# Kernel optimization log

Hardware: AMD Instinct MI355X
Metric: run time of the kernel (lower is better)

## Reference

```python
import jax, jax.numpy as jnp
import numpy as np

T, N, C_IN, M, ORDER = 16384, 16, 2, 3, 3
S = M * ORDER + ORDER + 1  # 13 weights per (out_ch, in_ch)


def setup_inputs() -> dict:
    key = jax.random.key(0)
    ks = jax.random.split(key, 6)
    return {
        "inputs": jax.random.normal(ks[0], (T, N, C_IN), jnp.float32),
        "a_list": jax.random.uniform(ks[1], (M, N, N), jnp.float32),  # positive -> valid D^{-1/2}
        "gcn_wx": 0.25 * jax.random.normal(ks[2], (T, C_IN, S), jnp.float32),
        "gcn_bx": jnp.zeros((T, N), jnp.float32),
        "gcn_wh": 0.25 * jax.random.normal(ks[3], (T, 1, S), jnp.float32),
        "gcn_bh": jnp.zeros((T, N), jnp.float32),
        "gru_k": 0.25 * jax.random.normal(ks[4], (T, 6, N, N), jnp.float32),  # Wr,Ur,Wz,Uz,Wh,Uh kernels
        "gru_b": jnp.zeros((T, 6, N), jnp.float32),
    }


def _laplacians(a_list):
    # Per motif: D = diag(colsum(A)); L = D - A; L_hat = D^{-1/2} L D^{-1/2}
    d = jnp.sum(a_list, axis=1)                      # [M,N] column sums (tf.reduce_sum axis=0)
    L = jax.vmap(jnp.diag)(d) - a_list               # [M,N,N]
    dis = 1.0 / jnp.sqrt(d)                          # diag of inv(sqrt(D))
    return dis[:, :, None] * L * dis[:, None, :]     # [M,N,N]


def _gcn(x, L_hats, W, b):
    # x: [N,C]; W: [C,S]; b: [N]. Chebyshev-style polynomial per input channel.
    I = jnp.eye(N, dtype=x.dtype)

    def per_channel(w):  # w: [S]
        ws = w[M * ORDER + 1] * I
        P = I
        for k in range(1, ORDER):
            coeffs = jnp.stack([w[l * (k - 1)] for l in range(M)])  # faithful odd indexing
            P = jnp.einsum('l,lij,jk->ik', coeffs, L_hats, P)
            ws = ws + w[M * ORDER + k + 1] * P
        return ws  # [N,N]

    WS = jax.vmap(per_channel)(W)                    # [C,N,N]
    out = jnp.einsum('cnm,mc->n', WS, x)             # sum_c WS[c] @ x[:,c]
    return jax.nn.relu(out + b)                      # [N] (N == 16 == bias width)


def _gru(x, h, K, B):
    # x, h: [N]; K: [6,N,N]; B: [6,N]
    r = jax.nn.sigmoid(x @ K[0] + B[0] + h @ K[1] + B[1])
    z = jax.nn.sigmoid(x @ K[2] + B[2] + h @ K[3] + B[3])
    hc = jnp.tanh(x @ K[4] + B[4] + (r * h) @ K[5] + B[5])
    return z * h + (1.0 - z) * hc


def reference(inputs, a_list, gcn_wx, gcn_bx, gcn_wh, gcn_bh, gru_k, gru_b):
    L_hats = _laplacians(a_list)

    # t == 0: hidden GCN branch is zeros
    xg0 = _gcn(inputs[0], L_hats, gcn_wx[0], gcn_bx[0])
    h0 = _gru(xg0, jnp.zeros((N,), inputs.dtype), gru_k[0], gru_b[0])

    def step(h_prev, per_t):
        x_t, wx, bx, wh, bh, K, B = per_t
        xg = _gcn(x_t, L_hats, wx, bx)
        hg = _gcn(h_prev[:, None], L_hats, wh, bh)   # hidden treated as [N,1] features
        h_t = _gru(xg, hg, K, B)
        return h_t, h_t

    xs = (inputs[1:], gcn_wx[1:], gcn_bx[1:], gcn_wh[1:], gcn_bh[1:], gru_k[1:], gru_b[1:])
    _, hs = jax.lax.scan(step, h0, xs)
    return jnp.concatenate([h0[None], hs], axis=0)   # [T, N]
```

## Files before the change

### kernel.cpp

```cpp
#include <hip/hip_runtime.h>

#define TT 16384
#define W_WARM 416
#define CHUNK 16
#define NSTEP (W_WARM + CHUNK)
#define RECF 1088
#define RECB 4352

#define RL(v, m) __int_as_float(__builtin_amdgcn_readlane(__float_as_int(v), (m)))
#define ROR(v, K) \
    __int_as_float(__builtin_amdgcn_update_dpp(0, __float_as_int(v), 0x120 + (K), 0xF, 0xF, false))

__device__ __forceinline__ float fsig(float x) {
    return __builtin_amdgcn_rcpf(1.0f + __builtin_amdgcn_exp2f(-1.4426950408889634f * x));
}
__device__ __forceinline__ float ftanh(float x) {
    return fmaf(-2.0f, __builtin_amdgcn_rcpf(1.0f + __builtin_amdgcn_exp2f(2.8853900817779268f * x)), 1.0f);
}

__global__ void k_fixed(const float* __restrict__ a, float* __restrict__ fix) {
    __shared__ float Lh[3][16][16];
    __shared__ float Ls[16][16];
    __shared__ float dsh[3][16];
    int tid = threadIdx.x;
    if (tid < 48) {
        int l = tid >> 4, j = tid & 15;
        float s = 0.f;
        for (int i = 0; i < 16; i++) s += a[l * 256 + i * 16 + j];
        dsh[l][j] = s;
    }
    __syncthreads();
    int i = tid >> 4, j = tid & 15;
    for (int l = 0; l < 3; l++) {
        float L = ((i == j) ? dsh[l][i] : 0.0f) - a[l * 256 + i * 16 + j];
        Lh[l][i][j] = L * rsqrtf(dsh[l][i]) * rsqrtf(dsh[l][j]);
    }
    __syncthreads();
    float ls = Lh[0][i][j] + Lh[1][i][j] + Lh[2][i][j];
    Ls[i][j] = ls;
    fix[i * 16 + j] = ls;
    __syncthreads();
    for (int l = 0; l < 3; l++) {
        float m = 0.f;
        for (int k = 0; k < 16; k++) m += Lh[l][i][k] * Ls[k][j];
        fix[(l + 1) * 256 + i * 16 + j] = m;
    }
}

__global__ __launch_bounds__(128) void k_prep3(const float* __restrict__ inp,
                                               const float* __restrict__ wx_,
                                               const float* __restrict__ bx_,
                                               const float* __restrict__ wh_,
                                               const float* __restrict__ bh_,
                                               const float* __restrict__ gk,
                                               const float* __restrict__ gb,
                                               float* __restrict__ ws) {
    __shared__ float sfix[1024];
    __shared__ float srec[8][RECF];
    __shared__ float sgk[8][768];
    __shared__ float sxg[8][16];
    int tid = threadIdx.x;
    int t_base = blockIdx.x * 8;
    for (int i = tid; i < 1024; i += 128) sfix[i] = ws[i];
    {
        float4* dst = (float4*)&sgk[0][0];
        const float4* src = (const float4*)gk;
        for (int i = tid; i < 1536; i += 128) {
            int tl2 = i / 192, r = i - tl2 * 192;
            int mtx = r >> 6, w = r & 63;
            dst[i] = src[(size_t)(t_base + tl2) * 384 + mtx * 128 + w];
        }
    }
    __syncthreads();
    int tl = tid >> 4, n = tid & 15;
    int t = t_base + tl;
    bool z0 = (t == 0);

    const float* wh = wh_ + t * 13;
    float w0 = wh[0];
    float aI = wh[10], aL = wh[11] * w0;
    float wc = wh[12] * w0;
    float c0 = wc * w0, c1 = wc * wh[1], c2 = wc * wh[2];
    for (int m = 0; m < 16; m++) {
        float Av = aL * sfix[n * 16 + m] + c0 * sfix[256 + n * 16 + m] +
                   c1 * sfix[512 + n * 16 + m] + c2 * sfix[768 + n * 16 + m];
        if (m == n) Av += aI;
        srec[tl][n * 16 + ((n - m) & 15)] = z0 ? 0.f : Av;
    }

    float acc = bx_[t * 16 + n];
    for (int c = 0; c < 2; c++) {
        const float* wx = wx_ + t * 26 + c * 13;
        float yL = 0.f, y0 = 0.f, y1 = 0.f, y2 = 0.f;
        for (int m = 0; m < 16; m++) {
            float xm = inp[t * 32 + m * 2 + c];
            yL += sfix[n * 16 + m] * xm;
            y0 += sfix[256 + n * 16 + m] * xm;
            y1 += sfix[512 + n * 16 + m] * xm;
            y2 += sfix[768 + n * 16 + m] * xm;
        }
        float xn = inp[t * 32 + n * 2 + c];
        float b0 = wx[12] * wx[0];
        acc += wx[10] * xn + wx[11] * wx[0] * yL + b0 * (wx[0] * y0 + wx[1] * y1 + wx[2] * y2);
    }
    float xg = fmaxf(acc, 0.f);
    sxg[tl][n] = xg;
    __syncthreads();

    const float* gbt = gb + (size_t)t * 96;
    float u[3];
    for (int qq = 0; qq < 3; qq++) {
        const float* K = &sgk[tl][qq * 256];
        float s = gbt[2 * qq * 16 + n] + gbt[(2 * qq + 1) * 16 + n];
        for (int m = 0; m < 16; m++) s += sxg[tl][m] * K[m * 16 + n];
        u[qq] = s;
    }
    srec[tl][1024 + n * 4 + 0] = z0 ? 0.f : bh_[t * 16 + n];
    srec[tl][1024 + n * 4 + 1] = u[0];
    srec[tl][1024 + n * 4 + 2] = u[1];
    srec[tl][1024 + n * 4 + 3] = u[2];
    __syncthreads();
    {
        float4* dst = (float4*)&sgk[0][0];
        const float4* src = (const float4*)gk;
        for (int i = tid; i < 1536; i += 128) {
            int tl2 = i / 192, r = i - tl2 * 192;
            int mtx = r >> 6, w = r & 63;
            dst[i] = src[(size_t)(t_base + tl2) * 384 + mtx * 128 + 64 + w];
        }
    }
    __syncthreads();
    for (int b = 0; b < 3; b++) {
        const float* K = &sgk[tl][b * 256];
        float* d = &srec[tl][256 * (b + 1)];
        for (int m = 0; m < 16; m++)
            d[n * 16 + ((n - m) & 15)] = K[m * 16 + n];
    }
    __syncthreads();
    float4* gdst = (float4*)(ws + 1024 + (size_t)t_base * RECF);
    const float4* lsrc = (const float4*)&srec[0][0];
    for (int i = tid; i < 8 * RECF / 4; i += 128) gdst[i] = lsrc[i];
}

struct Slot {
    float4 A0, A1, A2, A3;
    float4 B0, B1, B2, B3;
    float4 Z0, Z1, Z2, Z3;
    float4 C0, C1, C2, C3;
    float4 ex;
};

__device__ __forceinline__ void rot16(float v, float rr[16]) {
    rr[0] = v;
    rr[1] = ROR(v, 1);
    rr[2] = ROR(v, 2);
    rr[3] = ROR(v, 3);
    rr[4] = ROR(v, 4);
    rr[5] = ROR(v, 5);
    rr[6] = ROR(v, 6);
    rr[7] = ROR(v, 7);
    rr[8] = ROR(v, 8);
    rr[9] = ROR(v, 9);
    rr[10] = ROR(v, 10);
    rr[11] = ROR(v, 11);
    rr[12] = ROR(v, 12);
    rr[13] = ROR(v, 13);
    rr[14] = ROR(v, 14);
    rr[15] = ROR(v, 15);
}

__device__ __forceinline__ float dotw(const float4& w0, const float4& w1, const float4& w2,
                                      const float4& w3, const float rr[16]) {
    float a0 = w0.x * rr[0];
    float a1 = w0.y * rr[1];
    float a2 = w0.z * rr[2];
    float a3 = w0.w * rr[3];
    a0 = fmaf(w1.x, rr[4], a0);
    a1 = fmaf(w1.y, rr[5], a1);
    a2 = fmaf(w1.z, rr[6], a2);
    a3 = fmaf(w1.w, rr[7], a3);
    a0 = fmaf(w2.x, rr[8], a0);
    a1 = fmaf(w2.y, rr[9], a1);
    a2 = fmaf(w2.z, rr[10], a2);
    a3 = fmaf(w2.w, rr[11], a3);
    a0 = fmaf(w3.x, rr[12], a0);
    a1 = fmaf(w3.y, rr[13], a1);
    a2 = fmaf(w3.z, rr[14], a2);
    a3 = fmaf(w3.w, rr[15], a3);
    return (a0 + a1) + (a2 + a3);
}

__device__ __forceinline__ void load_slot(Slot& S, const char* __restrict__ recb8, int t,
                                          unsigned offA, unsigned offX) {
    const char* r = recb8 + (size_t)t * RECB;
    S.A0 = *(const float4*)(r + offA);
    S.A1 = *(const float4*)(r + offA + 16);
    S.A2 = *(const float4*)(r + offA + 32);
    S.A3 = *(const float4*)(r + offA + 48);
    S.B0 = *(const float4*)(r + offA + 1024);
    S.B1 = *(const float4*)(r + offA + 1040);
    S.B2 = *(const float4*)(r + offA + 1056);
    S.B3 = *(const float4*)(r + offA + 1072);
    S.Z0 = *(const float4*)(r + offA + 2048);
    S.Z1 = *(const float4*)(r + offA + 2064);
    S.Z2 = *(const float4*)(r + offA + 2080);
    S.Z3 = *(const float4*)(r + offA + 2096);
    S.C0 = *(const float4*)(r + offA + 3072);
    S.C1 = *(const float4*)(r + offA + 3088);
    S.C2 = *(const float4*)(r + offA + 3104);
    S.C3 = *(const float4*)(r + offA + 3120);
    S.ex = *(const float4*)(r + offX);
}

__device__ __forceinline__ float wstep6(const Slot& S, float hv, int t, int t0, int n,
                                        float* __restrict__ out) {
    float hh[16];
    rot16(hv, hh);
    float hg = fmaxf(dotw(S.A0, S.A1, S.A2, S.A3, hh) + S.ex.x, 0.f);
    float hgr[16];
    rot16(hg, hgr);
    float r = fsig(dotw(S.B0, S.B1, S.B2, S.B3, hgr) + S.ex.y);
    float z = fsig(dotw(S.Z0, S.Z1, S.Z2, S.Z3, hgr) + S.ex.z);
    float rg[16];
    rot16(r * hg, rg);
    float hc = ftanh(dotw(S.C0, S.C1, S.C2, S.C3, rg) + S.ex.w);
    float hn = fmaf(z, hg - hc, hc);
    if ((unsigned)(t - t0) < (unsigned)CHUNK) out[(size_t)t * 16 + n] = hn;
    return hn;
}

__global__ __launch_bounds__(64, 1) void k_walk6(const float* __restrict__ ws,
                                                 float* __restrict__ out) {
    const char* recb8 = (const char*)(ws + 1024);
    int lane = threadIdx.x;
    int n = lane & 15;
    int row = lane >> 4;

    unsigned offA = n * 64;
    unsigned offX = 4096 + n * 16;

    int b = blockIdx.x;
    int L = (b & 7) * 32 + (b >> 3);
    int t0 = (L * 4 + row) * CHUNK;
    int ts = t0 - W_WARM;
    if (ts < 0) ts = 0;
    int tend = t0 + CHUNK - 1;

    float hv = 0.f;

    Slot R0, R1, R2;
    load_slot(R0, recb8, ts + 0, offA, offX);
    load_slot(R1, recb8, ts + 1, offA, offX);
    load_slot(R2, recb8, ts + 2, offA, offX);

    for (int s = 0; s < NSTEP; s += 3) {
        int t = ts + s;
        int tl;
        hv = wstep6(R0, hv, t + 0, t0, n, out);
        tl = t + 3;
        if (tl > tend) tl = tend;
        load_slot(R0, recb8, tl, offA, offX);
        hv = wstep6(R1, hv, t + 1, t0, n, out);
        tl = t + 4;
        if (tl > tend) tl = tend;
        load_slot(R1, recb8, tl, offA, offX);
        hv = wstep6(R2, hv, t + 2, t0, n, out);
        tl = t + 5;
        if (tl > tend) tl = tend;
        load_slot(R2, recb8, tl, offA, offX);
    }
}

__global__ void k_prep_c(const float* __restrict__ inp, const float* __restrict__ wx_,
                         const float* __restrict__ bx_, const float* __restrict__ wh_,
                         const float* __restrict__ bh_, const float* __restrict__ gk,
                         const float* __restrict__ gb, float* __restrict__ ws) {
    __shared__ float sfix[1024];
    __shared__ float sxg[16][16];
    int tid = threadIdx.x;
    for (int idx = tid; idx < 1024; idx += 256) sfix[idx] = ws[idx];
    int tl = tid >> 4, n = tid & 15;
    int t = blockIdx.x * 16 + tl;
    __syncthreads();
    float* rec = ws + 1024 + (size_t)t * 320;
    bool z0 = (t == 0);
    const float* wh = wh_ + t * 13;
    float w0 = wh[0];
    float aI = wh[10], aL = wh[11] * w0;
    float wc = wh[12] * w0;
    float c0 = wc * w0, c1 = wc * wh[1], c2 = wc * wh[2];
    for (int m = 0; m < 16; m++) {
        float Av = aL * sfix[n * 16 + m] + c0 * sfix[256 + n * 16 + m] +
                   c1 * sfix[512 + n * 16 + m] + c2 * sfix[768 + n * 16 + m];
        if (m == n) Av += aI;
        rec[n * 16 + m] = z0 ? 0.f : Av;
    }
    float acc = bx_[t * 16 + n];
    for (int c = 0; c < 2; c++) {
        const float* wx = wx_ + t * 26 + c * 13;
        float yL = 0.f, y0 = 0.f, y1 = 0.f, y2 = 0.f;
        for (int m = 0; m < 16; m++) {
            float xm = inp[t * 32 + m * 2 + c];
            yL += sfix[n * 16 + m] * xm;
            y0 += sfix[256 + n * 16 + m] * xm;
            y1 += sfix[512 + n * 16 + m] * xm;
            y2 += sfix[768 + n * 16 + m] * xm;
        }
        float xn = inp[t * 32 + n * 2 + c];
        float b0 = wx[12] * wx[0];
        acc += wx[10] * xn + wx[11] * wx[0] * yL + b0 * (wx[0] * y0 + wx[1] * y1 + wx[2] * y2);
    }
    float xg = fmaxf(acc, 0.f);
    sxg[tl][n] = xg;
    __syncthreads();
    const float* Kb = gk + (size_t)t * 1536;
    const float* gbt = gb + (size_t)t * 96;
    for (int qq = 0; qq < 3; qq++) {
        const float* K = Kb + (2 * qq) * 256;
        float u = gbt[2 * qq * 16 + n] + gbt[(2 * qq + 1) * 16 + n];
        for (int m = 0; m < 16; m++) u += sxg[tl][m] * K[m * 16 + n];
        rec[256 + qq * 16 + n] = u;
    }
    rec[304 + n] = z0 ? 0.f : bh_[t * 16 + n];
}

struct RegsC {
    float WA[16], WB[16], WC[16];
    float uRZ, u4, bh;
};

__device__ __forceinline__ void load_step_c(const float* __restrict__ recb,
                                            const float* __restrict__ gk, int t, int n, int q,
                                            RegsC& R) {
    const float* rb = recb + (size_t)t * 320;
#pragma unroll
    for (int k = 0; k < 4; k++) ((float4*)R.WA)[k] = ((const float4*)(rb + n * 16))[k];
    const float* kb = gk + (size_t)t * 1536 + (1 + 2 * (q & 1)) * 256 + n;
    const float* kc = gk + (size_t)t * 1536 + 5 * 256 + n;
#pragma unroll
    for (int m = 0; m < 16; m++) {
        R.WB[m] = kb[m * 16];
        R.WC[m] = kc[m * 16];
    }
    R.uRZ = rb[256 + (q & 1) * 16 + n];
    R.u4 = rb[288 + n];
    R.bh = rb[304 + n];
}

__device__ __forceinline__ void wstep_c(const RegsC& R, float hs[16], int t, int t0, int lane,
                                        int n, float* __restrict__ out) {
    float a0 = 0.f, a1 = 0.f, a2 = 0.f, a3 = 0.f;
#pragma unroll
    for (int m = 0; m < 16; m += 4) {
        a0 = fmaf(R.WA[m + 0], hs[m + 0], a0);
        a1 = fmaf(R.WA[m + 1], hs[m + 1], a1);
        a2 = fmaf(R.WA[m + 2], hs[m + 2], a2);
        a3 = fmaf(R.WA[m + 3], hs[m + 3], a3);
    }
    float hg = fmaxf((a0 + a1) + (a2 + a3) + R.bh, 0.f);
    float hgs[16];
#pragma unroll
    for (int m = 0; m < 16; m++) hgs[m] = RL(hg, m);
    a0 = a1 = a2 = a3 = 0.f;
#pragma unroll
    for (int m = 0; m < 16; m += 4) {
        a0 = fmaf(R.WB[m + 0], hgs[m + 0], a0);
        a1 = fmaf(R.WB[m + 1], hgs[m + 1], a1);
        a2 = fmaf(R.WB[m + 2], hgs[m + 2], a2);
        a3 = fmaf(R.WB[m + 3], hgs[m + 3], a3);
    }
    float rz = fsig((a0 + a1) + (a2 + a3) + R.uRZ);
    float zsw = __shfl_xor(rz, 16);
    float rhg = rz * hg;
    float rhgs[16];
#pragma unroll
    for (int m = 0; m < 16; m++) rhgs[m] = RL(rhg, m);
    a0 = a1 = a2 = a3 = 0.f;
#pragma unroll
    for (int m = 0; m < 16; m += 4) {
        a0 = fmaf(R.WC[m + 0], rhgs[m + 0], a0);
        a1 = fmaf(R.WC[m + 1], rhgs[m + 1], a1);
        a2 = fmaf(R.WC[m + 2], rhgs[m + 2], a2);
        a3 = fmaf(R.WC[m + 3], rhgs[m + 3], a3);
    }
    float hc = ftanh((a0 + a1) + (a2 + a3) + R.u4);
    float h = fmaf(zsw, hg - hc, hc);
    if (t >= t0 && lane < 16) out[(size_t)t * 16 + n] = h;
#pragma unroll
    for (int m = 0; m < 16; m++) hs[m] = RL(h, m);
}

__global__ __launch_bounds__(64) void k_walk_c(const float* __restrict__ ws,
                                               const float* __restrict__ gk,
                                               float* __restrict__ out) {
    const float* recb = ws + 1024;
    int lane = threadIdx.x;
    int n = lane & 15;
    int q = lane >> 4;
    int t0 = blockIdx.x * 64;
    int te = t0 + 64;
    int ts = t0 - W_WARM;
    if (ts < 0) ts = 0;
    RegsC Ra, Rb;
    load_step_c(recb, gk, ts, n, q, Ra);
    load_step_c(recb, gk, ts + 1, n, q, Rb);
    float hs[16];
#pragma unroll
    for (int m = 0; m < 16; m++) hs[m] = 0.f;
    for (int t = ts; t < te; t += 2) {
        wstep_c(Ra, hs, t, t0, lane, n, out);
        int tn = t + 2;
        load_step_c(recb, gk, tn < TT ? tn : TT - 1, n, q, Ra);
        wstep_c(Rb, hs, t + 1, t0, lane, n, out);
        int tm = t + 3;
        load_step_c(recb, gk, tm < TT ? tm : TT - 1, n, q, Rb);
    }
}

extern "C" void kernel_launch(void* const* d_in, const int* in_sizes, int n_in, void* d_out,
                              int out_size, void* d_ws, size_t ws_size, hipStream_t stream) {
    const float* inp = (const float*)d_in[0];
    const float* a = (const float*)d_in[1];
    const float* wx = (const float*)d_in[2];
    const float* bx = (const float*)d_in[3];
    const float* wh = (const float*)d_in[4];
    const float* bh = (const float*)d_in[5];
    const float* gk = (const float*)d_in[6];
    const float* gb = (const float*)d_in[7];
    float* out = (float*)d_out;
    float* ws = (float*)d_ws;

    size_t need = 4ull * (1024ull + (size_t)TT * RECF);
    k_fixed<<<dim3(1), dim3(256), 0, stream>>>(a, ws);
    if (ws_size >= need) {
        k_prep3<<<dim3(TT / 8), dim3(128), 0, stream>>>(inp, wx, bx, wh, bh, gk, gb, ws);
        k_walk6<<<dim3(TT / (4 * CHUNK)), dim3(64), 0, stream>>>(ws, out);
    } else {
        k_prep_c<<<dim3(TT / 16), dim3(256), 0, stream>>>(inp, wx, bx, wh, bh, gk, gb, ws);
        k_walk_c<<<dim3(TT / 64), dim3(64), 0, stream>>>(ws, gk, out);
    }
}
```

Before: 506.7 us.

## Stream recurrence records through swizzled LDS ring with async global-to-LDS loads

Replaces direct global-to-register slot loads in the sequential walk with a 4-deep LDS ring filled by global_load_lds and read via ds_read_b128 with manual waitcnt control. Records are written with an XOR swizzle in prep to avoid LDS bank conflicts. Each block now walks two 32-step chains instead of four 16-step chains, reducing total redundant warmup work. Risks include fragile hand-tuned waitcnt counts and a slightly longer serial chain per block.

Result: no change. 500.8 us (-1.2%).

```diff
diff --git a/kernel.cpp b/kernel.cpp
--- a/kernel.cpp
+++ b/kernel.cpp
@@ -2,14 +2,22 @@
 
 #define TT 16384
 #define W_WARM 416
-#define CHUNK 16
+#define CHUNK 32
 #define NSTEP (W_WARM + CHUNK)
 #define RECF 1088
 #define RECB 4352
+#define NS 4
+#define SLOTF 2176
+#define SLOTB 8704
 
 #define RL(v, m) __int_as_float(__builtin_amdgcn_readlane(__float_as_int(v), (m)))
 #define ROR(v, K) \
     __int_as_float(__builtin_amdgcn_update_dpp(0, __float_as_int(v), 0x120 + (K), 0xF, 0xF, false))
+
+#define VMWAIT10() asm volatile("s_waitcnt vmcnt(10)")
+#define VMWAIT20() asm volatile("s_waitcnt vmcnt(20)")
+#define LGKMWAIT15() asm volatile("s_waitcnt lgkmcnt(15)")
+#define LAUNDER4(v) asm volatile("" : "+v"((v).x), "+v"((v).y), "+v"((v).z), "+v"((v).w))
 
 __device__ __forceinline__ float fsig(float x) {
     return __builtin_amdgcn_rcpf(1.0f + __builtin_amdgcn_exp2f(-1.4426950408889634f * x));
@@ -75,6 +83,7 @@
     int tl = tid >> 4, n = tid & 15;
     int t = t_base + tl;
     bool z0 = (t == 0);
+    int sw = (n >> 1) & 3;
 
     const float* wh = wh_ + t * 13;
     float w0 = wh[0];
@@ -85,7 +94,8 @@
         float Av = aL * sfix[n * 16 + m] + c0 * sfix[256 + n * 16 + m] +
                    c1 * sfix[512 + n * 16 + m] + c2 * sfix[768 + n * 16 + m];
         if (m == n) Av += aI;
-        srec[tl][n * 16 + ((n - m) & 15)] = z0 ? 0.f : Av;
+        int j = (n - m) & 15;
+        srec[tl][n * 16 + ((((j >> 2) ^ sw) << 2) | (j & 3))] = z0 ? 0.f : Av;
     }
 
     float acc = bx_[t * 16 + n];
@@ -133,8 +143,10 @@
     for (int b = 0; b < 3; b++) {
         const float* K = &sgk[tl][b * 256];
         float* d = &srec[tl][256 * (b + 1)];
-        for (int m = 0; m < 16; m++)
-            d[n * 16 + ((n - m) & 15)] = K[m * 16 + n];
+        for (int m = 0; m < 16; m++) {
+            int j = (n - m) & 15;
+            d[n * 16 + ((((j >> 2) ^ sw) << 2) | (j & 3))] = K[m * 16 + n];
+        }
     }
     __syncthreads();
     float4* gdst = (float4*)(ws + 1024 + (size_t)t_base * RECF);
@@ -142,13 +154,76 @@
     for (int i = tid; i < 8 * RECF / 4; i += 128) gdst[i] = lsrc[i];
 }
 
-struct Slot {
+struct SReg {
     float4 A0, A1, A2, A3;
     float4 B0, B1, B2, B3;
     float4 Z0, Z1, Z2, Z3;
     float4 C0, C1, C2, C3;
     float4 ex;
 };
+
+template <int OFF>
+__device__ __forceinline__ float4 dsr(unsigned a) {
+    float4 d;
+    asm volatile("ds_read_b128 %0, %1 offset:%2" : "=v"(d) : "v"(a), "i"(OFF));
+    return d;
+}
+
+template <int SLOT>
+__device__ __forceinline__ void read_slot(const unsigned aA[4], unsigned aex, SReg& R) {
+    constexpr int B = SLOT * SLOTB;
+    R.A0 = dsr<B>(aA[0]);
+    R.A1 = dsr<B>(aA[1]);
+    R.A2 = dsr<B>(aA[2]);
+    R.A3 = dsr<B>(aA[3]);
+    R.B0 = dsr<B + 1024>(aA[0]);
+    R.B1 = dsr<B + 1024>(aA[1]);
+    R.B2 = dsr<B + 1024>(aA[2]);
+    R.B3 = dsr<B + 1024>(aA[3]);
+    R.Z0 = dsr<B + 2048>(aA[0]);
+    R.Z1 = dsr<B + 2048>(aA[1]);
+    R.Z2 = dsr<B + 2048>(aA[2]);
+    R.Z3 = dsr<B + 2048>(aA[3]);
+    R.C0 = dsr<B + 3072>(aA[0]);
+    R.C1 = dsr<B + 3072>(aA[1]);
+    R.C2 = dsr<B + 3072>(aA[2]);
+    R.C3 = dsr<B + 3072>(aA[3]);
+    R.ex = dsr<B>(aex);
+}
+
+__device__ __forceinline__ void gate(SReg& R) {
+    LAUNDER4(R.A0);
+    LAUNDER4(R.A1);
+    LAUNDER4(R.A2);
+    LAUNDER4(R.A3);
+    LAUNDER4(R.B0);
+    LAUNDER4(R.B1);
+    LAUNDER4(R.B2);
+    LAUNDER4(R.B3);
+    LAUNDER4(R.Z0);
+    LAUNDER4(R.Z1);
+    LAUNDER4(R.Z2);
+    LAUNDER4(R.Z3);
+    LAUNDER4(R.C0);
+    LAUNDER4(R.C1);
+    LAUNDER4(R.C2);
+    LAUNDER4(R.C3);
+    LAUNDER4(R.ex);
+}
+
+__device__ __forceinline__ void fetch_rec(const float* __restrict__ g, unsigned loff, int lane) {
+    const float* gs = g + lane * 4;
+#pragma unroll
+    for (int i = 0; i < 4; i++)
+        __builtin_amdgcn_global_load_lds(
+            (const __attribute__((address_space(1))) unsigned int*)(gs + i * 256),
+            (__attribute__((address_space(3))) unsigned int*)(unsigned)(loff + i * 1024u), 16, 0,
+            0);
+    if (lane < 16)
+        __builtin_amdgcn_global_load_lds(
+            (const __attribute__((address_space(1))) unsigned int*)(gs + 1024),
+            (__attribute__((address_space(3))) unsigned int*)(unsigned)(loff + 4096u), 16, 0, 0);
+}
 
 __device__ __forceinline__ void rot16(float v, float rr[16]) {
     rr[0] = v;
@@ -190,30 +265,8 @@
     return (a0 + a1) + (a2 + a3);
 }
 
-__device__ __forceinline__ void load_slot(Slot& S, const char* __restrict__ recb8, int t,
-                                          unsigned offA, unsigned offX) {
-    const char* r = recb8 + (size_t)t * RECB;
-    S.A0 = *(const float4*)(r + offA);
-    S.A1 = *(const float4*)(r + offA + 16);
-    S.A2 = *(const float4*)(r + offA + 32);
-    S.A3 = *(const float4*)(r + offA + 48);
-    S.B0 = *(const float4*)(r + offA + 1024);
-    S.B1 = *(const float4*)(r + offA + 1040);
-    S.B2 = *(const float4*)(r + offA + 1056);
-    S.B3 = *(const float4*)(r + offA + 1072);
-    S.Z0 = *(const float4*)(r + offA + 2048);
-    S.Z1 = *(const float4*)(r + offA + 2064);
-    S.Z2 = *(const float4*)(r + offA + 2080);
-    S.Z3 = *(const float4*)(r + offA + 2096);
-    S.C0 = *(const float4*)(r + offA + 3072);
-    S.C1 = *(const float4*)(r + offA + 3088);
-    S.C2 = *(const float4*)(r + offA + 3104);
-    S.C3 = *(const float4*)(r + offA + 3120);
-    S.ex = *(const float4*)(r + offX);
-}
-
-__device__ __forceinline__ float wstep6(const Slot& S, float hv, int t, int t0, int n,
-                                        float* __restrict__ out) {
+__device__ __forceinline__ float wstep10(const SReg& S, float hv, int t, int t0, int lane, int n,
+                                         float* __restrict__ out) {
     float hh[16];
     rot16(hv, hh);
     float hg = fmaxf(dotw(S.A0, S.A1, S.A2, S.A3, hh) + S.ex.x, 0.f);
@@ -225,49 +278,82 @@
     rot16(r * hg, rg);
     float hc = ftanh(dotw(S.C0, S.C1, S.C2, S.C3, rg) + S.ex.w);
     float hn = fmaf(z, hg - hc, hc);
-    if ((unsigned)(t - t0) < (unsigned)CHUNK) out[(size_t)t * 16 + n] = hn;
+    if (!((lane >> 4) & 1) && (unsigned)(t - t0) < (unsigned)CHUNK)
+        out[(size_t)t * 16 + n] = hn;
     return hn;
 }
 
-__global__ __launch_bounds__(64, 1) void k_walk6(const float* __restrict__ ws,
-                                                 float* __restrict__ out) {
-    const char* recb8 = (const char*)(ws + 1024);
+template <int U>
+__device__ __forceinline__ void half_step(SReg& cur, SReg& nxt, int sU, const unsigned aA[4],
+                                          unsigned aex, const float* __restrict__ recb,
+                                          unsigned ring0, int tsa, int tsb, int tena, int tenb,
+                                          int lane, int n, int tsl, int t0l, float& hv,
+                                          float* __restrict__ out) {
+    VMWAIT10();
+    read_slot<(U + 1) & 3>(aA, aex, nxt);
+    LGKMWAIT15();
+    __builtin_amdgcn_sched_barrier(0);
+    gate(cur);
+    int tfa = tsa + sU + 3;
+    if (tfa > tena) tfa = tena;
+    int tfb = tsb + sU + 3;
+    if (tfb > tenb) tfb = tenb;
+    unsigned lo = ring0 + ((U + 3) & 3) * SLOTB;
+    fetch_rec(recb + (size_t)tfa * RECF, lo, lane);
+    fetch_rec(recb + (size_t)tfb * RECF, lo + 4352, lane);
+    hv = wstep10(cur, hv, tsl + sU, t0l, lane, n, out);
+}
+
+__global__ __launch_bounds__(64, 1) void k_walk10(const float* __restrict__ ws,
+                                                  float* __restrict__ out) {
+    __shared__ __align__(16) float ring[NS * SLOTF];
+    const float* recb = ws + 1024;
     int lane = threadIdx.x;
     int n = lane & 15;
-    int row = lane >> 4;
-
-    unsigned offA = n * 64;
-    unsigned offX = 4096 + n * 16;
+    int chain = lane >> 5;
+    int sw = (n >> 1) & 3;
+
+    unsigned ring0 = (unsigned)(unsigned long long)(void*)ring;
+    unsigned aA[4];
+#pragma unroll
+    for (int k = 0; k < 4; k++) aA[k] = ring0 + chain * 4352 + n * 64 + 16 * (k ^ sw);
+    unsigned aex = ring0 + chain * 4352 + 4096 + n * 16;
 
     int b = blockIdx.x;
     int L = (b & 7) * 32 + (b >> 3);
-    int t0 = (L * 4 + row) * CHUNK;
-    int ts = t0 - W_WARM;
-    if (ts < 0) ts = 0;
-    int tend = t0 + CHUNK - 1;
+    int t0a = (2 * L) * CHUNK, t0b = (2 * L + 1) * CHUNK;
+    int tsa = t0a - W_WARM;
+    if (tsa < 0) tsa = 0;
+    int tsb = t0b - W_WARM;
+    if (tsb < 0) tsb = 0;
+    int tena = t0a + CHUNK - 1, tenb = t0b + CHUNK - 1;
+    int t0l = chain ? t0b : t0a;
+    int tsl = chain ? tsb : tsa;
+
+#pragma unroll
+    for (int i = 0; i < 3; i++) {
+        unsigned lo = ring0 + i * SLOTB;
+        fetch_rec(recb + (size_t)(tsa + i) * RECF, lo, lane);
+        fetch_rec(recb + (size_t)(tsb + i) * RECF, lo + 4352, lane);
+    }
+    VMWAIT20();
+    SReg Ra, Rb;
+    read_slot<0>(aA, aex, Ra);
+    asm volatile("s_waitcnt lgkmcnt(0)");
+    __builtin_amdgcn_sched_barrier(0);
+    gate(Ra);
 
     float hv = 0.f;
 
-    Slot R0, R1, R2;
-    load_slot(R0, recb8, ts + 0, offA, offX);
-    load_slot(R1, recb8, ts + 1, offA, offX);
-    load_slot(R2, recb8, ts + 2, offA, offX);
-
-    for (int s = 0; s < NSTEP; s += 3) {
-        int t = ts + s;
-        int tl;
-        hv = wstep6(R0, hv, t + 0, t0, n, out);
-        tl = t + 3;
-        if (tl > tend) tl = tend;
-        load_slot(R0, recb8, tl, offA, offX);
-        hv = wstep6(R1, hv, t + 1, t0, n, out);
-        tl = t + 4;
-        if (tl > tend) tl = tend;
-        load_slot(R1, recb8, tl, offA, offX);
-        hv = wstep6(R2, hv, t + 2, t0, n, out);
-        tl = t + 5;
-        if (tl > tend) tl = tend;
-        load_slot(R2, recb8, tl, offA, offX);
+    for (int s = 0; s < NSTEP; s += 4) {
+        half_step<0>(Ra, Rb, s + 0, aA, aex, recb, ring0, tsa, tsb, tena, tenb, lane, n, tsl,
+                     t0l, hv, out);
+        half_step<1>(Rb, Ra, s + 1, aA, aex, recb, ring0, tsa, tsb, tena, tenb, lane, n, tsl,
+                     t0l, hv, out);
+        half_step<2>(Ra, Rb, s + 2, aA, aex, recb, ring0, tsa, tsb, tena, tenb, lane, n, tsl,
+                     t0l, hv, out);
+        half_step<3>(Rb, Ra, s + 3, aA, aex, recb, ring0, tsa, tsb, tena, tenb, lane, n, tsl,
+                     t0l, hv, out);
     }
 }
 
@@ -434,7 +520,7 @@
     k_fixed<<<dim3(1), dim3(256), 0, stream>>>(a, ws);
     if (ws_size >= need) {
         k_prep3<<<dim3(TT / 8), dim3(128), 0, stream>>>(inp, wx, bx, wh, bh, gk, gb, ws);
-        k_walk6<<<dim3(TT / (4 * CHUNK)), dim3(64), 0, stream>>>(ws, out);
+        k_walk10<<<dim3(TT / (2 * CHUNK)), dim3(64), 0, stream>>>(ws, out);
     } else {
         k_prep_c<<<dim3(TT / 16), dim3(256), 0, stream>>>(inp, wx, bx, wh, bh, gk, gb, ws);
         k_walk_c<<<dim3(TT / 64), dim3(64), 0, stream>>>(ws, gk, out);
```
